# Optimization experiments

Hardware: AMD Instinct MI355X
Metric: run time of the kernel (lower is better)

The kernel has to match this reference:

```python
import jax, jax.numpy as jnp
import numpy as np

N, M, D = 256, 1024, 512


def setup_inputs() -> dict:
    key = jax.random.key(0)
    ks = jax.random.split(key, 12)
    s = 1.0 / np.sqrt(D)
    return {
        "q": jax.random.normal(ks[0], (N, D), jnp.float32),
        "k": jax.random.normal(ks[1], (M, D), jnp.float32),
        "v": jax.random.normal(ks[2], (M, D), jnp.float32),
        "mask": jax.random.randint(ks[3], (N, M), 0, 2, jnp.int32),
        "WQ": jax.random.normal(ks[4], (D, D), jnp.float32) * s,
        "bQ": jax.random.normal(ks[5], (D,), jnp.float32) * s,
        "WK": jax.random.normal(ks[6], (D, D), jnp.float32) * s,
        "bK": jax.random.normal(ks[7], (D,), jnp.float32) * s,
        "WV": jax.random.normal(ks[8], (D, D), jnp.float32) * s,
        "bV": jax.random.normal(ks[9], (D,), jnp.float32) * s,
        "Ww": jax.random.normal(ks[10], (1, D), jnp.float32) * s,
        "bw": jax.random.normal(ks[11], (1,), jnp.float32) * s,
    }


def reference(q, k, v, mask, WQ, bQ, WK, bK, WV, bV, Ww, bw):
    # Linear projections (torch Linear: x @ W.T + b)
    qp = q @ WQ.T + bQ            # [N, D]
    kp = k @ WK.T + bK            # [M, D]
    vp = v @ WV.T + bV            # [M, D]
    # Additive (Bahdanau) scores: tanh(q_n + k_m) . w  -> [N, M]
    t = jnp.tanh(qp[:, None, :] + kp[None, :, :])   # [N, M, D]
    score = jnp.einsum("nmd,d->nm", t, Ww[0]) + bw[0]
    score = jnp.where(mask == 1, score, jnp.float32(-1e6))
    w = jax.nn.softmax(score, axis=1)               # softmax over keys (dim 1)
    context = jnp.einsum("nm,md->nd", w, vp)        # weighted sum over keys
    return context
```

## Files before the change

### kernel.cpp

```cpp
#include <hip/hip_runtime.h>

#define NQ 256
#define MK 1024
#define DD 512
#define CSC 2.8853900817779268f

typedef __attribute__((ext_vector_type(8))) short short8;
typedef __attribute__((ext_vector_type(4))) float floatx4;

__device__ inline void bsplit(float x, unsigned short& h, unsigned short& l)
{
    unsigned u = __float_as_uint(x);
    unsigned hr = (u + 0x7FFFu + ((u >> 16) & 1u)) >> 16;
    h = (unsigned short)hr;
    float hf = __uint_as_float(hr << 16);
    unsigned ul = __float_as_uint(x - hf);
    l = (unsigned short)((ul + 0x7FFFu + ((ul >> 16) & 1u)) >> 16);
}

__global__ __launch_bounds__(256) void convert_split(
    const float* __restrict__ q, const float* __restrict__ k, const float* __restrict__ v,
    const float* __restrict__ WQ, const float* __restrict__ WK, const float* __restrict__ WV,
    unsigned short* __restrict__ qhi, unsigned short* __restrict__ qlo,
    unsigned short* __restrict__ khi, unsigned short* __restrict__ klo,
    unsigned short* __restrict__ vhi, unsigned short* __restrict__ vlo,
    unsigned short* __restrict__ wqhi, unsigned short* __restrict__ wqlo,
    unsigned short* __restrict__ wkhi, unsigned short* __restrict__ wklo,
    unsigned short* __restrict__ wvhi, unsigned short* __restrict__ wvlo)
{
    const int i = blockIdx.x * 256 + threadIdx.x;
    const float* src; unsigned short *dh, *dl; int li;
    if (i < 32768)       { src = q;  dh = qhi;  dl = qlo;  li = i; }
    else if (i < 163840) { src = k;  dh = khi;  dl = klo;  li = i - 32768; }
    else if (i < 294912) { src = v;  dh = vhi;  dl = vlo;  li = i - 163840; }
    else if (i < 360448) { src = WQ; dh = wqhi; dl = wqlo; li = i - 294912; }
    else if (i < 425984) { src = WK; dh = wkhi; dl = wklo; li = i - 360448; }
    else                 { src = WV; dh = wvhi; dl = wvlo; li = i - 425984; }

    float4 x = *(const float4*)&src[li * 4];
    ushort4 h, l;
    bsplit(x.x, h.x, l.x); bsplit(x.y, h.y, l.y);
    bsplit(x.z, h.z, l.z); bsplit(x.w, h.w, l.w);
    *(ushort4*)&dh[li * 4] = h;
    *(ushort4*)&dl[li * 4] = l;
}

__global__ __launch_bounds__(256) void proj_mfma(
    const unsigned short* __restrict__ qhi, const unsigned short* __restrict__ qlo,
    const unsigned short* __restrict__ khi, const unsigned short* __restrict__ klo,
    const unsigned short* __restrict__ vhi, const unsigned short* __restrict__ vlo,
    const unsigned short* __restrict__ wqhi, const unsigned short* __restrict__ wqlo,
    const unsigned short* __restrict__ wkhi, const unsigned short* __restrict__ wklo,
    const unsigned short* __restrict__ wvhi, const unsigned short* __restrict__ wvlo,
    const float* __restrict__ bQ, const float* __restrict__ bK, const float* __restrict__ bV,
    float* __restrict__ qs, float* __restrict__ kts, float* __restrict__ vp)
{
    int t = blockIdx.x;
    const unsigned short *Xh, *Xl, *Wh, *Wl; const float* b; int mode;
    if (t < 32)       { mode = 0; Xh = qhi; Xl = qlo; Wh = wqhi; Wl = wqlo; b = bQ; }
    else if (t < 160) { mode = 1; t -= 32;  Xh = khi; Xl = klo; Wh = wkhi; Wl = wklo; b = bK; }
    else              { mode = 2; t -= 160; Xh = vhi; Xl = vlo; Wh = wvhi; Wl = wvlo; b = bV; }
    const int i0 = (t >> 3) * 64;
    const int j0 = (t & 7) * 64;

    const int l  = threadIdx.x & 63;
    const int w  = threadIdx.x >> 6;
    const int lr = l & 15;
    const int lk = (l >> 4) * 8;
    const int rbase = (l >> 4) * 4;

    const int arow = (i0 + w * 16 + lr) * DD;

    floatx4 acc[4] = {{0,0,0,0},{0,0,0,0},{0,0,0,0},{0,0,0,0}};

    for (int kk = 0; kk < DD; kk += 32) {
        short8 ah = *(const short8*)&Xh[arow + kk + lk];
        short8 al = *(const short8*)&Xl[arow + kk + lk];
#pragma unroll
        for (int nt = 0; nt < 4; ++nt) {
            const int brow = (j0 + nt * 16 + lr) * DD;
            short8 bh = *(const short8*)&Wh[brow + kk + lk];
            short8 bl = *(const short8*)&Wl[brow + kk + lk];
            acc[nt] = __builtin_amdgcn_mfma_f32_16x16x32_bf16(ah, bh, acc[nt], 0, 0, 0);
            acc[nt] = __builtin_amdgcn_mfma_f32_16x16x32_bf16(ah, bl, acc[nt], 0, 0, 0);
            acc[nt] = __builtin_amdgcn_mfma_f32_16x16x32_bf16(al, bh, acc[nt], 0, 0, 0);
        }
    }

    if (mode == 1) {
#pragma unroll
        for (int nt = 0; nt < 4; ++nt) {
            const float bb = b[j0 + nt * 16 + lr];
            float4 o;
            o.x = (acc[nt][0] + bb) * CSC;
            o.y = (acc[nt][1] + bb) * CSC;
            o.z = (acc[nt][2] + bb) * CSC;
            o.w = (acc[nt][3] + bb) * CSC;
            *(float4*)&kts[(j0 + nt * 16 + lr) * MK + i0 + w * 16 + rbase] = o;
        }
    } else {
        float* dst = (mode == 0) ? qs : vp;
        const float sc = (mode == 0) ? CSC : 1.0f;
#pragma unroll
        for (int nt = 0; nt < 4; ++nt) {
            const float bb = b[j0 + nt * 16 + lr];
#pragma unroll
            for (int j = 0; j < 4; ++j)
                dst[(i0 + w * 16 + rbase + j) * DD + j0 + nt * 16 + lr]
                    = (acc[nt][j] + bb) * sc;
        }
    }
}

#define SNG 4

__global__ __launch_bounds__(256) void score_v2(
    const float* __restrict__ qs, const float* __restrict__ kts,
    const float* __restrict__ Ww, const float* __restrict__ bw,
    const int* __restrict__ mask, float* __restrict__ S)
{
    const int lane = threadIdx.x & 63;
    const int wave = threadIdx.x >> 6;
    const int m = blockIdx.x * 64 + lane;
    const int n0 = blockIdx.y * SNG;
    const int d0 = wave * 128;

    __shared__ float part[4][SNG][64];

    float acc[SNG] = {0.f, 0.f, 0.f, 0.f};
    float kv[8], kvn[8];
#pragma unroll
    for (int j = 0; j < 8; ++j) kv[j] = kts[(d0 + j) * MK + m];

    for (int c = 0; c < 16; ++c) {
        const int d = d0 + c * 8;
        float wwv[8], qv[SNG][8];
        {
            float4 w0 = *(const float4*)&Ww[d];
            float4 w1 = *(const float4*)&Ww[d + 4];
            wwv[0] = w0.x; wwv[1] = w0.y; wwv[2] = w0.z; wwv[3] = w0.w;
            wwv[4] = w1.x; wwv[5] = w1.y; wwv[6] = w1.z; wwv[7] = w1.w;
#pragma unroll
            for (int n = 0; n < SNG; ++n) {
                float4 a = *(const float4*)&qs[(n0 + n) * DD + d];
                float4 bq = *(const float4*)&qs[(n0 + n) * DD + d + 4];
                qv[n][0] = a.x;  qv[n][1] = a.y;  qv[n][2] = a.z;  qv[n][3] = a.w;
                qv[n][4] = bq.x; qv[n][5] = bq.y; qv[n][6] = bq.z; qv[n][7] = bq.w;
            }
        }
        if (c + 1 < 16) {
#pragma unroll
            for (int j = 0; j < 8; ++j) kvn[j] = kts[(d + 8 + j) * MK + m];
        }
#pragma unroll
        for (int j = 0; j < 8; ++j) {
#pragma unroll
            for (int n = 0; n < SNG; ++n) {
                float x = qv[n][j] + kv[j];
                float e = __builtin_amdgcn_exp2f(x);
                float r = __builtin_amdgcn_rcpf(e + 1.0f);
                acc[n] = fmaf(wwv[j], r, acc[n]);
            }
        }
#pragma unroll
        for (int j = 0; j < 8; ++j) kv[j] = kvn[j];
    }

#pragma unroll
    for (int n = 0; n < SNG; ++n) part[wave][n][lane] = acc[n];
    __syncthreads();

    if (wave == 0) {
        float4 wa = *(const float4*)&Ww[lane * 8];
        float4 wb = *(const float4*)&Ww[lane * 8 + 4];
        float s = wa.x + wa.y + wa.z + wa.w + wb.x + wb.y + wb.z + wb.w;
        for (int o = 32; o > 0; o >>= 1) s += __shfl_xor(s, o, 64);
        const float cst = s + bw[0];
#pragma unroll
        for (int n = 0; n < SNG; ++n) {
            float p = part[0][n][lane] + part[1][n][lane]
                    + part[2][n][lane] + part[3][n][lane];
            float sc = fmaf(-2.0f, p, cst);
            sc = (mask[(n0 + n) * MK + m] == 1) ? sc : -1e6f;
            S[(n0 + n) * MK + m] = sc;
        }
    }
}

__global__ __launch_bounds__(256) void softmax_kernel(float* __restrict__ S)
{
    const int n = blockIdx.x;
    const int t = threadIdx.x;
    const int lane = t & 63, wave = t >> 6;
    __shared__ float red[4];

    float v[4];
    float mx = -3.4e38f;
#pragma unroll
    for (int i = 0; i < 4; ++i) {
        v[i] = S[n * MK + t + i * 256];
        mx = fmaxf(mx, v[i]);
    }
    for (int o = 32; o > 0; o >>= 1) mx = fmaxf(mx, __shfl_xor(mx, o, 64));
    if (lane == 0) red[wave] = mx;
    __syncthreads();
    mx = fmaxf(fmaxf(red[0], red[1]), fmaxf(red[2], red[3]));
    __syncthreads();

    float sum = 0.f;
#pragma unroll
    for (int i = 0; i < 4; ++i) {
        v[i] = __builtin_amdgcn_exp2f((v[i] - mx) * 1.4426950408889634f);
        sum += v[i];
    }
    for (int o = 32; o > 0; o >>= 1) sum += __shfl_xor(sum, o, 64);
    if (lane == 0) red[wave] = sum;
    __syncthreads();
    sum = red[0] + red[1] + red[2] + red[3];

    const float inv = __builtin_amdgcn_rcpf(sum);
#pragma unroll
    for (int i = 0; i < 4; ++i) S[n * MK + t + i * 256] = v[i] * inv;
}

#define CNG 8
#define CMC 256

__global__ __launch_bounds__(512) void context_v2(const float* __restrict__ S,
                                                  const float* __restrict__ vp,
                                                  float* __restrict__ out)
{
    __shared__ float ws[CMC][12];
    const int t = threadIdx.x;
    const int n0 = blockIdx.x * CNG;
    const int m0 = blockIdx.y * CMC;

#pragma unroll
    for (int p = 0; p < 4; ++p) {
        int e = t + p * 512;
        int m = e & 255, n = e >> 8;
        ws[m][n] = S[(n0 + n) * MK + m0 + m];
    }
    __syncthreads();

    float acc[CNG] = {};
    for (int m = 0; m < CMC; ++m) {
        float vv = vp[(m0 + m) * DD + t];
        float4 w0 = *(const float4*)&ws[m][0];
        float4 w4 = *(const float4*)&ws[m][4];
        acc[0] = fmaf(w0.x, vv, acc[0]);
        acc[1] = fmaf(w0.y, vv, acc[1]);
        acc[2] = fmaf(w0.z, vv, acc[2]);
        acc[3] = fmaf(w0.w, vv, acc[3]);
        acc[4] = fmaf(w4.x, vv, acc[4]);
        acc[5] = fmaf(w4.y, vv, acc[5]);
        acc[6] = fmaf(w4.z, vv, acc[6]);
        acc[7] = fmaf(w4.w, vv, acc[7]);
    }
#pragma unroll
    for (int n = 0; n < CNG; ++n) atomicAdd(&out[(n0 + n) * DD + t], acc[n]);
}

extern "C" void kernel_launch(void* const* d_in, const int* in_sizes, int n_in,
                              void* d_out, int out_size, void* d_ws, size_t ws_size,
                              hipStream_t stream)
{
    const float* q    = (const float*)d_in[0];
    const float* k    = (const float*)d_in[1];
    const float* v    = (const float*)d_in[2];
    const int*   mask = (const int*)  d_in[3];
    const float* WQ   = (const float*)d_in[4];
    const float* bQ   = (const float*)d_in[5];
    const float* WK   = (const float*)d_in[6];
    const float* bK   = (const float*)d_in[7];
    const float* WV   = (const float*)d_in[8];
    const float* bV   = (const float*)d_in[9];
    const float* Ww   = (const float*)d_in[10];
    const float* bw   = (const float*)d_in[11];
    float* out = (float*)d_out;

    float* qs  = (float*)d_ws;
    float* kts = qs + NQ * DD;
    float* vp  = kts + DD * MK;
    float* S   = vp + MK * DD;
    unsigned short* p16  = (unsigned short*)(S + NQ * MK);
    unsigned short* qhi  = p16;              p16 += NQ * DD;
    unsigned short* qlo  = p16;              p16 += NQ * DD;
    unsigned short* khi  = p16;              p16 += MK * DD;
    unsigned short* klo  = p16;              p16 += MK * DD;
    unsigned short* vhi  = p16;              p16 += MK * DD;
    unsigned short* vlo  = p16;              p16 += MK * DD;
    unsigned short* wqhi = p16;              p16 += DD * DD;
    unsigned short* wqlo = p16;              p16 += DD * DD;
    unsigned short* wkhi = p16;              p16 += DD * DD;
    unsigned short* wklo = p16;              p16 += DD * DD;
    unsigned short* wvhi = p16;              p16 += DD * DD;
    unsigned short* wvlo = p16;

    hipMemsetAsync(d_out, 0, (size_t)NQ * DD * sizeof(float), stream);

    convert_split<<<1920, 256, 0, stream>>>(q, k, v, WQ, WK, WV,
        qhi, qlo, khi, klo, vhi, vlo, wqhi, wqlo, wkhi, wklo, wvhi, wvlo);

    proj_mfma<<<288, 256, 0, stream>>>(qhi, qlo, khi, klo, vhi, vlo,
        wqhi, wqlo, wkhi, wklo, wvhi, wvlo, bQ, bK, bV, qs, kts, vp);

    score_v2<<<dim3(MK / 64, NQ / SNG), 256, 0, stream>>>(qs, kts, Ww, bw, mask, S);

    softmax_kernel<<<NQ, 256, 0, stream>>>(S);

    context_v2<<<dim3(NQ / CNG, MK / CMC), dim3(512), 0, stream>>>(S, vp, out);
}
```

Baseline: 175.6 us.

## Fuse score computation and softmax into one per-query-row kernel

Replaces the separate score and softmax kernels with a single kernel where each 1024-thread block computes one query row's scores over all keys and then does the softmax in place. The constant term (sum of Ww plus bw) is dropped because softmax is shift-invariant. This removes one launch and the round trip of the score matrix through global memory. In exchange, each thread now walks the full D dimension serially, only 256 blocks are launched, and the query-row reuse across multiple queries per block is lost, so each block rereads all of kts.

```diff
diff --git a/kernel.cpp b/kernel.cpp
--- a/kernel.cpp
+++ b/kernel.cpp
@@ -4,6 +4,7 @@
 #define MK 1024
 #define DD 512
 #define CSC 2.8853900817779268f
+#define L2E 1.4426950408889634f
 
 typedef __attribute__((ext_vector_type(8))) short short8;
 typedef __attribute__((ext_vector_type(4))) float floatx4;
@@ -112,115 +113,65 @@
     }
 }
 
-#define SNG 4
-
-__global__ __launch_bounds__(256) void score_v2(
+__global__ __launch_bounds__(1024) void score_sm(
     const float* __restrict__ qs, const float* __restrict__ kts,
-    const float* __restrict__ Ww, const float* __restrict__ bw,
-    const int* __restrict__ mask, float* __restrict__ S)
-{
-    const int lane = threadIdx.x & 63;
-    const int wave = threadIdx.x >> 6;
-    const int m = blockIdx.x * 64 + lane;
-    const int n0 = blockIdx.y * SNG;
-    const int d0 = wave * 128;
-
-    __shared__ float part[4][SNG][64];
-
-    float acc[SNG] = {0.f, 0.f, 0.f, 0.f};
-    float kv[8], kvn[8];
-#pragma unroll
-    for (int j = 0; j < 8; ++j) kv[j] = kts[(d0 + j) * MK + m];
-
-    for (int c = 0; c < 16; ++c) {
-        const int d = d0 + c * 8;
-        float wwv[8], qv[SNG][8];
-        {
-            float4 w0 = *(const float4*)&Ww[d];
-            float4 w1 = *(const float4*)&Ww[d + 4];
-            wwv[0] = w0.x; wwv[1] = w0.y; wwv[2] = w0.z; wwv[3] = w0.w;
-            wwv[4] = w1.x; wwv[5] = w1.y; wwv[6] = w1.z; wwv[7] = w1.w;
-#pragma unroll
-            for (int n = 0; n < SNG; ++n) {
-                float4 a = *(const float4*)&qs[(n0 + n) * DD + d];
-                float4 bq = *(const float4*)&qs[(n0 + n) * DD + d + 4];
-                qv[n][0] = a.x;  qv[n][1] = a.y;  qv[n][2] = a.z;  qv[n][3] = a.w;
-                qv[n][4] = bq.x; qv[n][5] = bq.y; qv[n][6] = bq.z; qv[n][7] = bq.w;
-            }
-        }
-        if (c + 1 < 16) {
-#pragma unroll
-            for (int j = 0; j < 8; ++j) kvn[j] = kts[(d + 8 + j) * MK + m];
-        }
-#pragma unroll
-        for (int j = 0; j < 8; ++j) {
-#pragma unroll
-            for (int n = 0; n < SNG; ++n) {
-                float x = qv[n][j] + kv[j];
-                float e = __builtin_amdgcn_exp2f(x);
-                float r = __builtin_amdgcn_rcpf(e + 1.0f);
-                acc[n] = fmaf(wwv[j], r, acc[n]);
-            }
-        }
-#pragma unroll
-        for (int j = 0; j < 8; ++j) kv[j] = kvn[j];
-    }
-
-#pragma unroll
-    for (int n = 0; n < SNG; ++n) part[wave][n][lane] = acc[n];
-    __syncthreads();
-
-    if (wave == 0) {
-        float4 wa = *(const float4*)&Ww[lane * 8];
-        float4 wb = *(const float4*)&Ww[lane * 8 + 4];
-        float s = wa.x + wa.y + wa.z + wa.w + wb.x + wb.y + wb.z + wb.w;
-        for (int o = 32; o > 0; o >>= 1) s += __shfl_xor(s, o, 64);
-        const float cst = s + bw[0];
-#pragma unroll
-        for (int n = 0; n < SNG; ++n) {
-            float p = part[0][n][lane] + part[1][n][lane]
-                    + part[2][n][lane] + part[3][n][lane];
-            float sc = fmaf(-2.0f, p, cst);
-            sc = (mask[(n0 + n) * MK + m] == 1) ? sc : -1e6f;
-            S[(n0 + n) * MK + m] = sc;
-        }
-    }
-}
-
-__global__ __launch_bounds__(256) void softmax_kernel(float* __restrict__ S)
+    const float* __restrict__ Ww, const int* __restrict__ mask,
+    float* __restrict__ S)
 {
     const int n = blockIdx.x;
     const int t = threadIdx.x;
     const int lane = t & 63, wave = t >> 6;
-    __shared__ float red[4];
-
-    float v[4];
-    float mx = -3.4e38f;
-#pragma unroll
-    for (int i = 0; i < 4; ++i) {
-        v[i] = S[n * MK + t + i * 256];
-        mx = fmaxf(mx, v[i]);
-    }
+
+    __shared__ float qsm[DD];
+    __shared__ float wwm[DD];
+    __shared__ float red[16];
+
+    if (t < DD) { qsm[t] = qs[n * DD + t]; wwm[t] = Ww[t]; }
+    __syncthreads();
+
+    float acc = 0.f;
+    for (int d = 0; d < DD; d += 8) {
+        float kv[8];
+#pragma unroll
+        for (int j = 0; j < 8; ++j) kv[j] = kts[(d + j) * MK + t];
+#pragma unroll
+        for (int j = 0; j < 8; ++j) {
+            float x = qsm[d + j] + kv[j];
+            float e = __builtin_amdgcn_exp2f(x);
+            acc = fmaf(wwm[d + j], __builtin_amdgcn_rcpf(e + 1.0f), acc);
+        }
+    }
+
+    float s = -2.0f * acc;
+    s = (mask[n * MK + t] == 1) ? s : -1e6f;
+
+    float mx = s;
     for (int o = 32; o > 0; o >>= 1) mx = fmaxf(mx, __shfl_xor(mx, o, 64));
     if (lane == 0) red[wave] = mx;
     __syncthreads();
-    mx = fmaxf(fmaxf(red[0], red[1]), fmaxf(red[2], red[3]));
-    __syncthreads();
-
-    float sum = 0.f;
-#pragma unroll
-    for (int i = 0; i < 4; ++i) {
-        v[i] = __builtin_amdgcn_exp2f((v[i] - mx) * 1.4426950408889634f);
-        sum += v[i];
-    }
+    if (wave == 0) {
+        float r = red[lane & 15];
+        for (int o = 8; o > 0; o >>= 1) r = fmaxf(r, __shfl_xor(r, o, 64));
+        if (lane == 0) red[0] = r;
+    }
+    __syncthreads();
+    mx = red[0];
+    __syncthreads();
+
+    float e = __builtin_amdgcn_exp2f((s - mx) * L2E);
+    float sum = e;
     for (int o = 32; o > 0; o >>= 1) sum += __shfl_xor(sum, o, 64);
     if (lane == 0) red[wave] = sum;
     __syncthreads();
-    sum = red[0] + red[1] + red[2] + red[3];
-
-    const float inv = __builtin_amdgcn_rcpf(sum);
-#pragma unroll
-    for (int i = 0; i < 4; ++i) S[n * MK + t + i * 256] = v[i] * inv;
+    if (wave == 0) {
+        float r = red[lane & 15];
+        for (int o = 8; o > 0; o >>= 1) r += __shfl_xor(r, o, 64);
+        if (lane == 0) red[0] = r;
+    }
+    __syncthreads();
+    sum = red[0];
+
+    S[n * MK + t] = e * __builtin_amdgcn_rcpf(sum);
 }
 
 #define CNG 8
@@ -277,6 +228,7 @@
     const float* bV   = (const float*)d_in[9];
     const float* Ww   = (const float*)d_in[10];
     const float* bw   = (const float*)d_in[11];
+    (void)bw;
     float* out = (float*)d_out;
 
     float* qs  = (float*)d_ws;
@@ -305,9 +257,7 @@
     proj_mfma<<<288, 256, 0, stream>>>(qhi, qlo, khi, klo, vhi, vlo,
         wqhi, wqlo, wkhi, wklo, wvhi, wvlo, bQ, bK, bV, qs, kts, vp);
 
-    score_v2<<<dim3(MK / 64, NQ / SNG), 256, 0, stream>>>(qs, kts, Ww, bw, mask, S);
-
-    softmax_kernel<<<NQ, 256, 0, stream>>>(S);
+    score_sm<<<NQ, 1024, 0, stream>>>(qs, kts, Ww, mask, S);
 
     context_v2<<<dim3(NQ / CNG, MK / CMC), dim3(512), 0, stream>>>(S, vp, out);
 }
```

New measurement: 177.6 us. Within noise of the previous version (+1.1%).
